# Optimization experiments

Hardware: AMD Instinct MI355X
Metric: run time of the kernel (lower is better)

The kernel has to match this reference:

```python
import jax, jax.numpy as jnp
import numpy as np

B, F, P = 16384, 4096, 32
D = F // P
EPS = 1e-5


def setup_inputs() -> dict:
    key = jax.random.key(0)
    ks = jax.random.split(key, 5)
    bound = 1.0 / np.sqrt(D)
    return {
        "x": jax.random.normal(ks[0], (B, F), dtype=jnp.float32),
        "weights1": jax.random.uniform(ks[1], (P, D, D), dtype=jnp.float32, minval=-bound, maxval=bound),
        "bias1": jax.random.uniform(ks[2], (F,), dtype=jnp.float32, minval=-bound, maxval=bound),
        "weights2": jax.random.uniform(ks[3], (P, D, D), dtype=jnp.float32, minval=-bound, maxval=bound),
        "bias2": jax.random.uniform(ks[4], (F,), dtype=jnp.float32, minval=-bound, maxval=bound),
        "gamma1": jnp.ones((F,), dtype=jnp.float32),
        "beta1": jnp.zeros((F,), dtype=jnp.float32),
        "gamma3": jnp.ones((F,), dtype=jnp.float32),
        "beta3": jnp.zeros((F,), dtype=jnp.float32),
    }


def _block_matmul(x, w):
    # x: [B, F] viewed as [B, P, D]; w: [P, D, D] block-diagonal blocks.
    # Equivalent to x @ block_diag(*w) without building the [F, F] matrix.
    xb = x.reshape(x.shape[0], P, D)
    return jnp.einsum("bpd,pde->bpe", xb, w).reshape(x.shape[0], F)


def _batchnorm(y, gamma, beta):
    # Training-mode BatchNorm1d: biased variance over the batch dim.
    mean = jnp.mean(y, axis=0)
    var = jnp.var(y, axis=0)
    return gamma * (y - mean) * jax.lax.rsqrt(var + EPS) + beta


def reference(x, weights1, bias1, weights2, bias2, gamma1, beta1, gamma3, beta3):
    o1 = jnp.tanh(_batchnorm(_block_matmul(x, weights1) + bias1, gamma1, beta1))
    o2 = _block_matmul(o1, weights2) + bias2
    o3 = jnp.tanh(_batchnorm(o2 + x, gamma3, beta3))
    return o3
```

## Files before the change

### kernel.cpp

```cpp
#include <hip/hip_runtime.h>
#include <hip/hip_bf16.h>
#include <cstdint>
#include <cstddef>

#define B_ 16384
#define F_ 4096
#define P_ 32
#define D_ 128
#define STRIPS 32
#define ITERS 8

using f32x4 = __attribute__((ext_vector_type(4))) float;
using s16x8 = __attribute__((ext_vector_type(8))) short;

union abuf { s16x8 v; uint32_t u[4]; };

__device__ inline uint32_t pk_bf16(float a, float b) {
    float2 f; f.x = a; f.y = b;
    union { __hip_bfloat162 h; uint32_t u; } cv;
    cv.h = __float22bfloat162_rn(f);
    return cv.u;
}
__device__ inline unsigned short bf16_rn1(float f) {
    union { float f; uint32_t u; } v; v.f = f;
    return (unsigned short)((v.u + 0x7FFFu + ((v.u >> 16) & 1u)) >> 16);
}
__device__ inline float bf16_f32(unsigned short h) {
    union { uint32_t u; float f; } v; v.u = ((uint32_t)h) << 16;
    return v.f;
}
__device__ inline float tanh_e(float ze) {
    float e = __builtin_amdgcn_exp2f(ze);
    return 1.f - 2.f * __builtin_amdgcn_rcpf(e + 1.f);
}

__device__ inline void stage_w(const float* __restrict__ Wp, short* s_w, int tid) {
#pragma unroll
    for (int it = 0; it < 8; ++it) {
        int slot = it * 256 + tid;
        int l15 = slot & 15;
        int l4  = (slot >> 4) & 3;
        int s   = (slot >> 6) & 3;
        int j   = slot >> 8;
        const float* src = Wp + (size_t)(s * 32 + l4 * 8) * D_ + j * 16 + l15;
        abuf a;
#pragma unroll
        for (int q = 0; q < 4; ++q) {
            float w0 = src[(size_t)(2 * q) * D_];
            float w1 = src[(size_t)(2 * q + 1) * D_];
            a.u[q] = pk_bf16(w0, w1);
        }
        *(s16x8*)((char*)s_w + (size_t)slot * 16) = a.v;
    }
}

template<bool OB>
__global__ __launch_bounds__(256, 4) void k_gemm1(
    const float* __restrict__ x, const float* __restrict__ W1,
    float* __restrict__ y1f, unsigned short* __restrict__ y1h,
    float* __restrict__ gsum, float* __restrict__ gsq)
{
    __shared__ short s_w[D_ * D_];
    __shared__ float s_sum[D_], s_sq[D_];
    const int tid = threadIdx.x;
    const int p = blockIdx.x / STRIPS;
    const int strip = blockIdx.x % STRIPS;
    stage_w(W1 + (size_t)p * D_ * D_, s_w, tid);
    if (tid < D_) { s_sum[tid] = 0.f; s_sq[tid] = 0.f; }
    __syncthreads();

    const int wave = tid >> 6, lane = tid & 63;
    const int l15 = lane & 15, l4 = lane >> 4;
    const int ldsb = lane * 16;

    float csum[8], csq[8];
#pragma unroll
    for (int j = 0; j < 8; ++j) { csum[j] = 0.f; csq[j] = 0.f; }

    for (int it = 0; it < ITERS; ++it) {
        const int row0 = strip * (ITERS * 64) + it * 64 + wave * 16;
        const float* ap = x + (size_t)(row0 + l15) * F_ + p * D_ + l4 * 8;
        f32x4 v[4][2];
#pragma unroll
        for (int s = 0; s < 4; ++s) {
            v[s][0] = *(const f32x4*)(ap + s * 32);
            v[s][1] = *(const f32x4*)(ap + s * 32 + 4);
        }
        abuf a[4];
#pragma unroll
        for (int s = 0; s < 4; ++s) {
            a[s].u[0] = pk_bf16(v[s][0][0], v[s][0][1]);
            a[s].u[1] = pk_bf16(v[s][0][2], v[s][0][3]);
            a[s].u[2] = pk_bf16(v[s][1][0], v[s][1][1]);
            a[s].u[3] = pk_bf16(v[s][1][2], v[s][1][3]);
        }
        f32x4 acc[8];
#pragma unroll
        for (int j = 0; j < 8; ++j) acc[j] = (f32x4){0.f, 0.f, 0.f, 0.f};
#pragma unroll
        for (int s = 0; s < 4; ++s)
#pragma unroll
            for (int j = 0; j < 8; ++j) {
                s16x8 b = *(const s16x8*)((const char*)s_w + (j * 4 + s) * 1024 + ldsb);
                acc[j] = __builtin_amdgcn_mfma_f32_16x16x32_bf16(a[s].v, b, acc[j], 0, 0, 0);
            }
        const int rb = row0 + l4 * 4;
#pragma unroll
        for (int j = 0; j < 8; ++j) {
            const size_t off = (size_t)rb * F_ + p * D_ + j * 16 + l15;
#pragma unroll
            for (int r = 0; r < 4; ++r) {
                float vv = acc[j][r];
                if (OB) y1h[off + (size_t)r * F_] = bf16_rn1(vv);
                else    y1f[off + (size_t)r * F_] = vv;
                csum[j] += vv;
                csq[j] = fmaf(vv, vv, csq[j]);
            }
        }
    }
#pragma unroll
    for (int j = 0; j < 8; ++j) {
        float sm = csum[j], q = csq[j];
        sm += __shfl_xor(sm, 16); q += __shfl_xor(q, 16);
        sm += __shfl_xor(sm, 32); q += __shfl_xor(q, 32);
        if (l4 == 0) {
            atomicAdd(&s_sum[j * 16 + l15], sm);
            atomicAdd(&s_sq[j * 16 + l15], q);
        }
    }
    __syncthreads();
    if (tid < D_) {
        atomicAdd(&gsum[p * D_ + tid], s_sum[tid]);
        atomicAdd(&gsq[p * D_ + tid], s_sq[tid]);
    }
}

template<bool IOB>
__global__ __launch_bounds__(256, 4) void k_gemm2(
    const float* __restrict__ x, float* __restrict__ yf,
    unsigned short* __restrict__ yh, const float* __restrict__ W2,
    const float* __restrict__ sce, const float* __restrict__ she,
    float* __restrict__ gsum, float* __restrict__ gsq)
{
    __shared__ short s_w[D_ * D_];
    __shared__ float s_sc[D_], s_sh[D_];
    __shared__ float s_sum[D_], s_sq[D_];
    const int tid = threadIdx.x;
    const int p = blockIdx.x / STRIPS;
    const int strip = blockIdx.x % STRIPS;
    stage_w(W2 + (size_t)p * D_ * D_, s_w, tid);
    if (tid < D_) {
        s_sc[tid] = sce[p * D_ + tid];
        s_sh[tid] = she[p * D_ + tid];
        s_sum[tid] = 0.f; s_sq[tid] = 0.f;
    }
    __syncthreads();

    const int wave = tid >> 6, lane = tid & 63;
    const int l15 = lane & 15, l4 = lane >> 4;
    const int ldsb = lane * 16;

    float csum[8], csq[8];
#pragma unroll
    for (int j = 0; j < 8; ++j) { csum[j] = 0.f; csq[j] = 0.f; }

    for (int it = 0; it < ITERS; ++it) {
        const int row0 = strip * (ITERS * 64) + it * 64 + wave * 16;
        s16x8 hv[4];
        f32x4 v[4][2];
        if (IOB) {
            const unsigned short* ap = yh + (size_t)(row0 + l15) * F_ + p * D_ + l4 * 8;
#pragma unroll
            for (int s = 0; s < 4; ++s) hv[s] = *(const s16x8*)(ap + s * 32);
        } else {
            const float* ap = yf + (size_t)(row0 + l15) * F_ + p * D_ + l4 * 8;
#pragma unroll
            for (int s = 0; s < 4; ++s) {
                v[s][0] = *(const f32x4*)(ap + s * 32);
                v[s][1] = *(const f32x4*)(ap + s * 32 + 4);
            }
        }
        abuf a[4];
#pragma unroll
        for (int s = 0; s < 4; ++s) {
            const int kb = s * 32 + l4 * 8;
            f32x4 sc0 = *(const f32x4*)&s_sc[kb];
            f32x4 sc1 = *(const f32x4*)&s_sc[kb + 4];
            f32x4 sh0 = *(const f32x4*)&s_sh[kb];
            f32x4 sh1 = *(const f32x4*)&s_sh[kb + 4];
            float t[8];
#pragma unroll
            for (int q = 0; q < 4; ++q) {
                float i0 = IOB ? bf16_f32((unsigned short)hv[s][q])     : v[s][0][q];
                float i1 = IOB ? bf16_f32((unsigned short)hv[s][q + 4]) : v[s][1][q];
                t[q]     = tanh_e(fmaf(i0, sc0[q], sh0[q]));
                t[q + 4] = tanh_e(fmaf(i1, sc1[q], sh1[q]));
            }
            a[s].u[0] = pk_bf16(t[0], t[1]);
            a[s].u[1] = pk_bf16(t[2], t[3]);
            a[s].u[2] = pk_bf16(t[4], t[5]);
            a[s].u[3] = pk_bf16(t[6], t[7]);
        }
        f32x4 acc[8];
#pragma unroll
        for (int j = 0; j < 8; ++j) acc[j] = (f32x4){0.f, 0.f, 0.f, 0.f};
#pragma unroll
        for (int s = 0; s < 4; ++s)
#pragma unroll
            for (int j = 0; j < 8; ++j) {
                s16x8 b = *(const s16x8*)((const char*)s_w + (j * 4 + s) * 1024 + ldsb);
                acc[j] = __builtin_amdgcn_mfma_f32_16x16x32_bf16(a[s].v, b, acc[j], 0, 0, 0);
            }
        const int rb = row0 + l4 * 4;
#pragma unroll
        for (int j = 0; j < 8; ++j) {
            const size_t off = (size_t)rb * F_ + p * D_ + j * 16 + l15;
#pragma unroll
            for (int r = 0; r < 4; ++r) {
                float vv = acc[j][r] + x[off + (size_t)r * F_];
                if (IOB) yh[off + (size_t)r * F_] = bf16_rn1(vv);
                else     yf[off + (size_t)r * F_] = vv;
                csum[j] += vv;
                csq[j] = fmaf(vv, vv, csq[j]);
            }
        }
    }
#pragma unroll
    for (int j = 0; j < 8; ++j) {
        float sm = csum[j], q = csq[j];
        sm += __shfl_xor(sm, 16); q += __shfl_xor(q, 16);
        sm += __shfl_xor(sm, 32); q += __shfl_xor(q, 32);
        if (l4 == 0) {
            atomicAdd(&s_sum[j * 16 + l15], sm);
            atomicAdd(&s_sq[j * 16 + l15], q);
        }
    }
    __syncthreads();
    if (tid < D_) {
        atomicAdd(&gsum[p * D_ + tid], s_sum[tid]);
        atomicAdd(&gsq[p * D_ + tid], s_sq[tid]);
    }
}

__global__ void k_finalize(const float* __restrict__ sum,
                           const float* __restrict__ sumsq,
                           const float* __restrict__ gamma,
                           const float* __restrict__ beta,
                           float* __restrict__ sce,
                           float* __restrict__ she)
{
    const float L2E2 = 2.f * 1.44269504088896340736f;
    int f = blockIdx.x * blockDim.x + threadIdx.x;
    if (f < F_) {
        float mean = sum[f] * (1.f / B_);
        float var  = sumsq[f] * (1.f / B_) - mean * mean;
        float rstd = rsqrtf(var + 1e-5f);
        float sc = gamma[f] * rstd;
        sce[f] = L2E2 * sc;
        she[f] = L2E2 * (beta[f] - mean * sc);
    }
}

template<bool IB>
__global__ void k_bn_tanh(const unsigned short* __restrict__ y3h,
                          float* __restrict__ outf,
                          const float* __restrict__ sce,
                          const float* __restrict__ she)
{
    if (IB) {
        const size_t n8 = (size_t)B_ * F_ / 8;
        size_t i = (size_t)blockIdx.x * blockDim.x + threadIdx.x;
        const size_t stride = (size_t)gridDim.x * blockDim.x;
        for (; i < n8; i += stride) {
            s16x8 hv = ((const s16x8*)y3h)[i];
            int col = (int)((i * 8) & (F_ - 1));
            f32x4 sc0 = *(const f32x4*)(sce + col);
            f32x4 sc1 = *(const f32x4*)(sce + col + 4);
            f32x4 sh0 = *(const f32x4*)(she + col);
            f32x4 sh1 = *(const f32x4*)(she + col + 4);
            f32x4 r0, r1;
#pragma unroll
            for (int t = 0; t < 4; ++t) {
                r0[t] = tanh_e(fmaf(bf16_f32((unsigned short)hv[t]),     sc0[t], sh0[t]));
                r1[t] = tanh_e(fmaf(bf16_f32((unsigned short)hv[t + 4]), sc1[t], sh1[t]));
            }
            ((f32x4*)outf)[i * 2]     = r0;
            ((f32x4*)outf)[i * 2 + 1] = r1;
        }
    } else {
        const size_t n4 = (size_t)B_ * F_ / 4;
        size_t i = (size_t)blockIdx.x * blockDim.x + threadIdx.x;
        const size_t stride = (size_t)gridDim.x * blockDim.x;
        for (; i < n4; i += stride) {
            f32x4 v = ((const f32x4*)outf)[i];
            int col = (int)((i * 4) & (F_ - 1));
            f32x4 sc = *(const f32x4*)(sce + col);
            f32x4 sh = *(const f32x4*)(she + col);
            f32x4 r;
#pragma unroll
            for (int t = 0; t < 4; ++t) r[t] = tanh_e(fmaf(v[t], sc[t], sh[t]));
            ((f32x4*)outf)[i] = r;
        }
    }
}

extern "C" void kernel_launch(void* const* d_in, const int* in_sizes, int n_in,
                              void* d_out, int out_size, void* d_ws, size_t ws_size,
                              hipStream_t stream) {
    const float* x      = (const float*)d_in[0];
    const float* W1     = (const float*)d_in[1];
    const float* W2     = (const float*)d_in[3];
    const float* gamma1 = (const float*)d_in[5];
    const float* beta1  = (const float*)d_in[6];
    const float* gamma3 = (const float*)d_in[7];
    const float* beta3  = (const float*)d_in[8];

    float* yf = (float*)d_out;
    float* S  = (float*)d_ws;
    float* sum1   = S;
    float* sumsq1 = S + 4096;
    float* sum3   = S + 8192;
    float* sumsq3 = S + 12288;
    float* sce1   = S + 16384;
    float* she1   = S + 20480;
    float* sce3   = S + 24576;
    float* she3   = S + 28672;
    unsigned short* yh = (unsigned short*)((char*)d_ws + 128 * 1024);

    const bool big = ws_size >= (size_t)128 * 1024 + (size_t)B_ * F_ * 2;

    hipMemsetAsync(d_ws, 0, 4 * 4096 * sizeof(float), stream);

    if (big) {
        k_gemm1<true><<<P_ * STRIPS, 256, 0, stream>>>(x, W1, yf, yh, sum1, sumsq1);
        k_finalize<<<F_ / 256, 256, 0, stream>>>(sum1, sumsq1, gamma1, beta1, sce1, she1);
        k_gemm2<true><<<P_ * STRIPS, 256, 0, stream>>>(x, yf, yh, W2, sce1, she1, sum3, sumsq3);
        k_finalize<<<F_ / 256, 256, 0, stream>>>(sum3, sumsq3, gamma3, beta3, sce3, she3);
        k_bn_tanh<true><<<2048, 256, 0, stream>>>(yh, yf, sce3, she3);
    } else {
        k_gemm1<false><<<P_ * STRIPS, 256, 0, stream>>>(x, W1, yf, yh, sum1, sumsq1);
        k_finalize<<<F_ / 256, 256, 0, stream>>>(sum1, sumsq1, gamma1, beta1, sce1, she1);
        k_gemm2<false><<<P_ * STRIPS, 256, 0, stream>>>(x, yf, yh, W2, sce1, she1, sum3, sumsq3);
        k_finalize<<<F_ / 256, 256, 0, stream>>>(sum3, sumsq3, gamma3, beta3, sce3, she3);
        k_bn_tanh<false><<<2048, 256, 0, stream>>>(yh, yf, sce3, she3);
    }
}
```

Measured before the change: 655.6 us.

## Store intermediates in MFMA-fragment tiled bf16 layout and move BN stats to separate kernel

The GEMM kernels now swap MFMA operand order so each lane holds four contiguous output columns. Intermediate bf16 activations are written as whole 16-byte fragments in a tiled layout that the next GEMM reads back directly, replacing the scattered 2-byte strided stores. The per-column sum and sum-of-squares reductions are removed from the GEMM epilogues and computed by a new dedicated stats kernel that re-reads the intermediate. This adds two launches and an extra pass over the intermediate, but in exchange gives coalesced, vectorized stores and lighter GEMM epilogues.

```diff
diff --git a/kernel.cpp b/kernel.cpp
--- a/kernel.cpp
+++ b/kernel.cpp
@@ -21,10 +21,6 @@
     cv.h = __float22bfloat162_rn(f);
     return cv.u;
 }
-__device__ inline unsigned short bf16_rn1(float f) {
-    union { float f; uint32_t u; } v; v.f = f;
-    return (unsigned short)((v.u + 0x7FFFu + ((v.u >> 16) & 1u)) >> 16);
-}
 __device__ inline float bf16_f32(unsigned short h) {
     union { uint32_t u; float f; } v; v.u = ((uint32_t)h) << 16;
     return v.f;
@@ -34,7 +30,7 @@
     return 1.f - 2.f * __builtin_amdgcn_rcpf(e + 1.f);
 }
 
-__device__ inline void stage_w(const float* __restrict__ Wp, short* s_w, int tid) {
+__device__ inline void stage_w1(const float* __restrict__ Wp, short* s_w, int tid) {
 #pragma unroll
     for (int it = 0; it < 8; ++it) {
         int slot = it * 256 + tid;
@@ -45,54 +41,63 @@
         const float* src = Wp + (size_t)(s * 32 + l4 * 8) * D_ + j * 16 + l15;
         abuf a;
 #pragma unroll
-        for (int q = 0; q < 4; ++q) {
-            float w0 = src[(size_t)(2 * q) * D_];
-            float w1 = src[(size_t)(2 * q + 1) * D_];
-            a.u[q] = pk_bf16(w0, w1);
-        }
+        for (int q = 0; q < 4; ++q)
+            a.u[q] = pk_bf16(src[(size_t)(2 * q) * D_], src[(size_t)(2 * q + 1) * D_]);
         *(s16x8*)((char*)s_w + (size_t)slot * 16) = a.v;
     }
 }
 
-template<bool OB>
+__device__ inline void stage_w2(const float* __restrict__ Wp, short* s_w, int tid) {
+#pragma unroll
+    for (int it = 0; it < 8; ++it) {
+        int slot = it * 256 + tid;
+        int l15 = slot & 15;
+        int l4  = (slot >> 4) & 3;
+        int sp  = (slot >> 6) & 3;
+        int j   = slot >> 8;
+        const float* s0 = Wp + (size_t)(sp * 32 + l4 * 4) * D_ + j * 16 + l15;
+        const float* s1 = s0 + (size_t)16 * D_;
+        abuf a;
+        a.u[0] = pk_bf16(s0[0],            s0[(size_t)D_]);
+        a.u[1] = pk_bf16(s0[(size_t)2*D_], s0[(size_t)3*D_]);
+        a.u[2] = pk_bf16(s1[0],            s1[(size_t)D_]);
+        a.u[3] = pk_bf16(s1[(size_t)2*D_], s1[(size_t)3*D_]);
+        *(s16x8*)((char*)s_w + (size_t)slot * 16) = a.v;
+    }
+}
+
+
+template<bool BH>
 __global__ __launch_bounds__(256, 4) void k_gemm1(
     const float* __restrict__ x, const float* __restrict__ W1,
-    float* __restrict__ y1f, unsigned short* __restrict__ y1h,
-    float* __restrict__ gsum, float* __restrict__ gsq)
+    float* __restrict__ yf, unsigned short* __restrict__ yh)
 {
     __shared__ short s_w[D_ * D_];
-    __shared__ float s_sum[D_], s_sq[D_];
     const int tid = threadIdx.x;
-    const int p = blockIdx.x / STRIPS;
-    const int strip = blockIdx.x % STRIPS;
-    stage_w(W1 + (size_t)p * D_ * D_, s_w, tid);
-    if (tid < D_) { s_sum[tid] = 0.f; s_sq[tid] = 0.f; }
+    const int p = blockIdx.x / STRIPS, strip = blockIdx.x % STRIPS;
+    stage_w1(W1 + (size_t)p * D_ * D_, s_w, tid);
     __syncthreads();
-
     const int wave = tid >> 6, lane = tid & 63;
     const int l15 = lane & 15, l4 = lane >> 4;
     const int ldsb = lane * 16;
 
-    float csum[8], csq[8];
-#pragma unroll
-    for (int j = 0; j < 8; ++j) { csum[j] = 0.f; csq[j] = 0.f; }
-
     for (int it = 0; it < ITERS; ++it) {
-        const int row0 = strip * (ITERS * 64) + it * 64 + wave * 16;
-        const float* ap = x + (size_t)(row0 + l15) * F_ + p * D_ + l4 * 8;
-        f32x4 v[4][2];
+        const int g = strip * 32 + it * 4 + wave;
+        const int row = g * 16 + l15;
+        const float* ap = x + (size_t)row * F_ + p * D_ + l4 * 8;
+        f32x4 v0[4], v1[4];
 #pragma unroll
         for (int s = 0; s < 4; ++s) {
-            v[s][0] = *(const f32x4*)(ap + s * 32);
-            v[s][1] = *(const f32x4*)(ap + s * 32 + 4);
+            v0[s] = *(const f32x4*)(ap + s * 32);
+            v1[s] = *(const f32x4*)(ap + s * 32 + 4);
         }
         abuf a[4];
 #pragma unroll
         for (int s = 0; s < 4; ++s) {
-            a[s].u[0] = pk_bf16(v[s][0][0], v[s][0][1]);
-            a[s].u[1] = pk_bf16(v[s][0][2], v[s][0][3]);
-            a[s].u[2] = pk_bf16(v[s][1][0], v[s][1][1]);
-            a[s].u[3] = pk_bf16(v[s][1][2], v[s][1][3]);
+            a[s].u[0] = pk_bf16(v0[s][0], v0[s][1]);
+            a[s].u[1] = pk_bf16(v0[s][2], v0[s][3]);
+            a[s].u[2] = pk_bf16(v1[s][0], v1[s][1]);
+            a[s].u[3] = pk_bf16(v1[s][2], v1[s][3]);
         }
         f32x4 acc[8];
 #pragma unroll
@@ -101,144 +106,182 @@
         for (int s = 0; s < 4; ++s)
 #pragma unroll
             for (int j = 0; j < 8; ++j) {
-                s16x8 b = *(const s16x8*)((const char*)s_w + (j * 4 + s) * 1024 + ldsb);
-                acc[j] = __builtin_amdgcn_mfma_f32_16x16x32_bf16(a[s].v, b, acc[j], 0, 0, 0);
-            }
-        const int rb = row0 + l4 * 4;
-#pragma unroll
-        for (int j = 0; j < 8; ++j) {
-            const size_t off = (size_t)rb * F_ + p * D_ + j * 16 + l15;
-#pragma unroll
-            for (int r = 0; r < 4; ++r) {
-                float vv = acc[j][r];
-                if (OB) y1h[off + (size_t)r * F_] = bf16_rn1(vv);
-                else    y1f[off + (size_t)r * F_] = vv;
-                csum[j] += vv;
-                csq[j] = fmaf(vv, vv, csq[j]);
-            }
-        }
-    }
-#pragma unroll
-    for (int j = 0; j < 8; ++j) {
-        float sm = csum[j], q = csq[j];
-        sm += __shfl_xor(sm, 16); q += __shfl_xor(q, 16);
-        sm += __shfl_xor(sm, 32); q += __shfl_xor(q, 32);
-        if (l4 == 0) {
-            atomicAdd(&s_sum[j * 16 + l15], sm);
-            atomicAdd(&s_sq[j * 16 + l15], q);
-        }
-    }
-    __syncthreads();
-    if (tid < D_) {
-        atomicAdd(&gsum[p * D_ + tid], s_sum[tid]);
-        atomicAdd(&gsq[p * D_ + tid], s_sq[tid]);
-    }
-}
-
-template<bool IOB>
+                s16x8 w = *(const s16x8*)((const char*)s_w + (j * 4 + s) * 1024 + ldsb);
+                acc[j] = __builtin_amdgcn_mfma_f32_16x16x32_bf16(w, a[s].v, acc[j], 0, 0, 0);
+            }
+        if (BH) {
+            unsigned short* tp = yh + ((size_t)g * 32 + p) * 2048 + lane * 8;
+#pragma unroll
+            for (int jp = 0; jp < 4; ++jp) {
+                abuf o;
+                o.u[0] = pk_bf16(acc[2*jp][0],   acc[2*jp][1]);
+                o.u[1] = pk_bf16(acc[2*jp][2],   acc[2*jp][3]);
+                o.u[2] = pk_bf16(acc[2*jp+1][0], acc[2*jp+1][1]);
+                o.u[3] = pk_bf16(acc[2*jp+1][2], acc[2*jp+1][3]);
+                *(s16x8*)(tp + jp * 512) = o.v;
+            }
+        } else {
+            float* rp = yf + (size_t)row * F_ + p * D_ + l4 * 4;
+#pragma unroll
+            for (int j = 0; j < 8; ++j) *(f32x4*)(rp + j * 16) = acc[j];
+        }
+    }
+}
+
+template<bool BH>
 __global__ __launch_bounds__(256, 4) void k_gemm2(
     const float* __restrict__ x, float* __restrict__ yf,
     unsigned short* __restrict__ yh, const float* __restrict__ W2,
-    const float* __restrict__ sce, const float* __restrict__ she,
-    float* __restrict__ gsum, float* __restrict__ gsq)
+    const float* __restrict__ sce, const float* __restrict__ she)
 {
     __shared__ short s_w[D_ * D_];
     __shared__ float s_sc[D_], s_sh[D_];
-    __shared__ float s_sum[D_], s_sq[D_];
     const int tid = threadIdx.x;
-    const int p = blockIdx.x / STRIPS;
-    const int strip = blockIdx.x % STRIPS;
-    stage_w(W2 + (size_t)p * D_ * D_, s_w, tid);
+    const int p = blockIdx.x / STRIPS, strip = blockIdx.x % STRIPS;
+    stage_w2(W2 + (size_t)p * D_ * D_, s_w, tid);
     if (tid < D_) {
         s_sc[tid] = sce[p * D_ + tid];
         s_sh[tid] = she[p * D_ + tid];
-        s_sum[tid] = 0.f; s_sq[tid] = 0.f;
     }
     __syncthreads();
-
     const int wave = tid >> 6, lane = tid & 63;
     const int l15 = lane & 15, l4 = lane >> 4;
     const int ldsb = lane * 16;
 
-    float csum[8], csq[8];
-#pragma unroll
-    for (int j = 0; j < 8; ++j) { csum[j] = 0.f; csq[j] = 0.f; }
-
     for (int it = 0; it < ITERS; ++it) {
-        const int row0 = strip * (ITERS * 64) + it * 64 + wave * 16;
-        s16x8 hv[4];
-        f32x4 v[4][2];
-        if (IOB) {
-            const unsigned short* ap = yh + (size_t)(row0 + l15) * F_ + p * D_ + l4 * 8;
-#pragma unroll
-            for (int s = 0; s < 4; ++s) hv[s] = *(const s16x8*)(ap + s * 32);
+        const int g = strip * 32 + it * 4 + wave;
+        const int row = g * 16 + l15;
+        abuf a[4];
+        if (BH) {
+            const unsigned short* tp = yh + ((size_t)g * 32 + p) * 2048 + lane * 8;
+            s16x8 hv[4];
+#pragma unroll
+            for (int sp = 0; sp < 4; ++sp) hv[sp] = *(const s16x8*)(tp + sp * 512);
+#pragma unroll
+            for (int sp = 0; sp < 4; ++sp) {
+                const int kb = sp * 32 + l4 * 4;
+                f32x4 sc0 = *(const f32x4*)&s_sc[kb], sc1 = *(const f32x4*)&s_sc[kb + 16];
+                f32x4 sh0 = *(const f32x4*)&s_sh[kb], sh1 = *(const f32x4*)&s_sh[kb + 16];
+                float t0[4], t1[4];
+#pragma unroll
+                for (int q = 0; q < 4; ++q) {
+                    t0[q] = tanh_e(fmaf(bf16_f32((unsigned short)hv[sp][q]),     sc0[q], sh0[q]));
+                    t1[q] = tanh_e(fmaf(bf16_f32((unsigned short)hv[sp][q + 4]), sc1[q], sh1[q]));
+                }
+                a[sp].u[0] = pk_bf16(t0[0], t0[1]);
+                a[sp].u[1] = pk_bf16(t0[2], t0[3]);
+                a[sp].u[2] = pk_bf16(t1[0], t1[1]);
+                a[sp].u[3] = pk_bf16(t1[2], t1[3]);
+            }
         } else {
-            const float* ap = yf + (size_t)(row0 + l15) * F_ + p * D_ + l4 * 8;
-#pragma unroll
-            for (int s = 0; s < 4; ++s) {
-                v[s][0] = *(const f32x4*)(ap + s * 32);
-                v[s][1] = *(const f32x4*)(ap + s * 32 + 4);
-            }
-        }
-        abuf a[4];
-#pragma unroll
-        for (int s = 0; s < 4; ++s) {
-            const int kb = s * 32 + l4 * 8;
-            f32x4 sc0 = *(const f32x4*)&s_sc[kb];
-            f32x4 sc1 = *(const f32x4*)&s_sc[kb + 4];
-            f32x4 sh0 = *(const f32x4*)&s_sh[kb];
-            f32x4 sh1 = *(const f32x4*)&s_sh[kb + 4];
-            float t[8];
-#pragma unroll
-            for (int q = 0; q < 4; ++q) {
-                float i0 = IOB ? bf16_f32((unsigned short)hv[s][q])     : v[s][0][q];
-                float i1 = IOB ? bf16_f32((unsigned short)hv[s][q + 4]) : v[s][1][q];
-                t[q]     = tanh_e(fmaf(i0, sc0[q], sh0[q]));
-                t[q + 4] = tanh_e(fmaf(i1, sc1[q], sh1[q]));
-            }
-            a[s].u[0] = pk_bf16(t[0], t[1]);
-            a[s].u[1] = pk_bf16(t[2], t[3]);
-            a[s].u[2] = pk_bf16(t[4], t[5]);
-            a[s].u[3] = pk_bf16(t[6], t[7]);
+            const float* ap = yf + (size_t)row * F_ + p * D_;
+#pragma unroll
+            for (int sp = 0; sp < 4; ++sp) {
+                const int kb = sp * 32 + l4 * 4;
+                f32x4 w0 = *(const f32x4*)(ap + kb);
+                f32x4 w1 = *(const f32x4*)(ap + kb + 16);
+                f32x4 sc0 = *(const f32x4*)&s_sc[kb], sc1 = *(const f32x4*)&s_sc[kb + 16];
+                f32x4 sh0 = *(const f32x4*)&s_sh[kb], sh1 = *(const f32x4*)&s_sh[kb + 16];
+                float t0[4], t1[4];
+#pragma unroll
+                for (int q = 0; q < 4; ++q) {
+                    t0[q] = tanh_e(fmaf(w0[q], sc0[q], sh0[q]));
+                    t1[q] = tanh_e(fmaf(w1[q], sc1[q], sh1[q]));
+                }
+                a[sp].u[0] = pk_bf16(t0[0], t0[1]);
+                a[sp].u[1] = pk_bf16(t0[2], t0[3]);
+                a[sp].u[2] = pk_bf16(t1[0], t1[1]);
+                a[sp].u[3] = pk_bf16(t1[2], t1[3]);
+            }
         }
         f32x4 acc[8];
 #pragma unroll
         for (int j = 0; j < 8; ++j) acc[j] = (f32x4){0.f, 0.f, 0.f, 0.f};
 #pragma unroll
-        for (int s = 0; s < 4; ++s)
+        for (int sp = 0; sp < 4; ++sp)
 #pragma unroll
             for (int j = 0; j < 8; ++j) {
-                s16x8 b = *(const s16x8*)((const char*)s_w + (j * 4 + s) * 1024 + ldsb);
-                acc[j] = __builtin_amdgcn_mfma_f32_16x16x32_bf16(a[s].v, b, acc[j], 0, 0, 0);
-            }
-        const int rb = row0 + l4 * 4;
+                s16x8 w = *(const s16x8*)((const char*)s_w + (j * 4 + sp) * 1024 + ldsb);
+                acc[j] = __builtin_amdgcn_mfma_f32_16x16x32_bf16(w, a[sp].v, acc[j], 0, 0, 0);
+            }
+        const float* xp = x + (size_t)row * F_ + p * D_ + l4 * 4;
 #pragma unroll
         for (int j = 0; j < 8; ++j) {
-            const size_t off = (size_t)rb * F_ + p * D_ + j * 16 + l15;
-#pragma unroll
-            for (int r = 0; r < 4; ++r) {
-                float vv = acc[j][r] + x[off + (size_t)r * F_];
-                if (IOB) yh[off + (size_t)r * F_] = bf16_rn1(vv);
-                else     yf[off + (size_t)r * F_] = vv;
-                csum[j] += vv;
-                csq[j] = fmaf(vv, vv, csq[j]);
-            }
-        }
-    }
-#pragma unroll
-    for (int j = 0; j < 8; ++j) {
-        float sm = csum[j], q = csq[j];
-        sm += __shfl_xor(sm, 16); q += __shfl_xor(q, 16);
-        sm += __shfl_xor(sm, 32); q += __shfl_xor(q, 32);
-        if (l4 == 0) {
-            atomicAdd(&s_sum[j * 16 + l15], sm);
-            atomicAdd(&s_sq[j * 16 + l15], q);
-        }
-    }
-    __syncthreads();
-    if (tid < D_) {
-        atomicAdd(&gsum[p * D_ + tid], s_sum[tid]);
-        atomicAdd(&gsq[p * D_ + tid], s_sq[tid]);
+            f32x4 xr = *(const f32x4*)(xp + j * 16);
+#pragma unroll
+            for (int r = 0; r < 4; ++r) acc[j][r] += xr[r];
+        }
+        if (BH) {
+            unsigned short* tp = yh + ((size_t)g * 32 + p) * 2048 + lane * 8;
+#pragma unroll
+            for (int jp = 0; jp < 4; ++jp) {
+                abuf o;
+                o.u[0] = pk_bf16(acc[2*jp][0],   acc[2*jp][1]);
+                o.u[1] = pk_bf16(acc[2*jp][2],   acc[2*jp][3]);
+                o.u[2] = pk_bf16(acc[2*jp+1][0], acc[2*jp+1][1]);
+                o.u[3] = pk_bf16(acc[2*jp+1][2], acc[2*jp+1][3]);
+                *(s16x8*)(tp + jp * 512) = o.v;
+            }
+        } else {
+            float* rp = yf + (size_t)row * F_ + p * D_ + l4 * 4;
+#pragma unroll
+            for (int j = 0; j < 8; ++j) *(f32x4*)(rp + j * 16) = acc[j];
+        }
+    }
+}
+
+template<bool BH>
+__global__ void k_stats(const float* __restrict__ yf,
+                        const unsigned short* __restrict__ yh,
+                        float* __restrict__ gsum, float* __restrict__ gsq)
+{
+    if (BH) {
+        const int tid = threadIdx.x;
+        const int p = blockIdx.x & 31, seg = blockIdx.x >> 5;
+        const int jp = tid >> 6, l4 = (tid >> 4) & 3, l15 = tid & 15;
+        const unsigned short* base = yh + (size_t)p * 2048 + jp * 512 + (l4 * 16 + l15) * 8;
+        float cs[8], cq[8];
+#pragma unroll
+        for (int t = 0; t < 8; ++t) { cs[t] = 0.f; cq[t] = 0.f; }
+        for (int g = seg * 128; g < seg * 128 + 128; ++g) {
+            s16x8 hv = *(const s16x8*)(base + (size_t)g * 65536);
+#pragma unroll
+            for (int t = 0; t < 8; ++t) {
+                float f = bf16_f32((unsigned short)hv[t]);
+                cs[t] += f; cq[t] = fmaf(f, f, cq[t]);
+            }
+        }
+#pragma unroll
+        for (int t = 0; t < 8; ++t) {
+            cs[t] += __shfl_xor(cs[t], 1); cq[t] += __shfl_xor(cq[t], 1);
+            cs[t] += __shfl_xor(cs[t], 2); cq[t] += __shfl_xor(cq[t], 2);
+            cs[t] += __shfl_xor(cs[t], 4); cq[t] += __shfl_xor(cq[t], 4);
+            cs[t] += __shfl_xor(cs[t], 8); cq[t] += __shfl_xor(cq[t], 8);
+        }
+        if (l15 == 0) {
+#pragma unroll
+            for (int t = 0; t < 8; ++t) {
+                int c = p * 128 + jp * 32 + (t >= 4 ? 16 : 0) + l4 * 4 + (t & 3);
+                atomicAdd(&gsum[c], cs[t]);
+                atomicAdd(&gsq[c],  cq[t]);
+            }
+        }
+    } else {
+        const int id = blockIdx.x * 256 + threadIdx.x;
+        const int c4 = id & 1023;
+        const int r0 = id >> 10;
+        const float* bp = yf + (size_t)r0 * F_ + c4 * 4;
+        f32x4 cs = {0.f,0.f,0.f,0.f}, cq = {0.f,0.f,0.f,0.f};
+        for (int k = 0; k < 64; ++k) {
+            f32x4 v = *(const f32x4*)(bp + (size_t)k * 256 * F_);
+#pragma unroll
+            for (int t = 0; t < 4; ++t) { cs[t] += v[t]; cq[t] = fmaf(v[t], v[t], cq[t]); }
+        }
+#pragma unroll
+        for (int t = 0; t < 4; ++t) {
+            atomicAdd(&gsum[c4 * 4 + t], cs[t]);
+            atomicAdd(&gsq[c4 * 4 + t],  cq[t]);
+        }
     }
 }
 
@@ -246,8 +289,7 @@
                            const float* __restrict__ sumsq,
                            const float* __restrict__ gamma,
                            const float* __restrict__ beta,
-                           float* __restrict__ sce,
-                           float* __restrict__ she)
+                           float* __restrict__ sce, float* __restrict__ she)
 {
     const float L2E2 = 2.f * 1.44269504088896340736f;
     int f = blockIdx.x * blockDim.x + threadIdx.x;
@@ -261,45 +303,49 @@
     }
 }
 
-template<bool IB>
-__global__ void k_bn_tanh(const unsigned short* __restrict__ y3h,
-                          float* __restrict__ outf,
+template<bool BH>
+__global__ void k_bn_tanh(const unsigned short* __restrict__ yh,
+                          float* __restrict__ out,
                           const float* __restrict__ sce,
                           const float* __restrict__ she)
 {
-    if (IB) {
-        const size_t n8 = (size_t)B_ * F_ / 8;
-        size_t i = (size_t)blockIdx.x * blockDim.x + threadIdx.x;
+    if (BH) {
+        const size_t NU = (size_t)B_ / 16 * P_ * 256;
+        size_t idx = (size_t)blockIdx.x * blockDim.x + threadIdx.x;
         const size_t stride = (size_t)gridDim.x * blockDim.x;
-        for (; i < n8; i += stride) {
-            s16x8 hv = ((const s16x8*)y3h)[i];
-            int col = (int)((i * 8) & (F_ - 1));
-            f32x4 sc0 = *(const f32x4*)(sce + col);
-            f32x4 sc1 = *(const f32x4*)(sce + col + 4);
-            f32x4 sh0 = *(const f32x4*)(she + col);
-            f32x4 sh1 = *(const f32x4*)(she + col + 4);
+        for (; idx < NU; idx += stride) {
+            s16x8 hv = *(const s16x8*)(yh + idx * 8);
+            int g = (int)(idx >> 13);
+            int rem = (int)(idx & 8191);
+            int p = rem >> 8, s = rem & 255;
+            int jp = s >> 6, l4 = (s >> 4) & 3, l15 = s & 15;
+            int c0 = p * 128 + jp * 32 + l4 * 4;
+            int row = g * 16 + l15;
+            f32x4 sc0 = *(const f32x4*)(sce + c0), sc1 = *(const f32x4*)(sce + c0 + 16);
+            f32x4 sh0 = *(const f32x4*)(she + c0), sh1 = *(const f32x4*)(she + c0 + 16);
             f32x4 r0, r1;
 #pragma unroll
             for (int t = 0; t < 4; ++t) {
                 r0[t] = tanh_e(fmaf(bf16_f32((unsigned short)hv[t]),     sc0[t], sh0[t]));
                 r1[t] = tanh_e(fmaf(bf16_f32((unsigned short)hv[t + 4]), sc1[t], sh1[t]));
             }
-            ((f32x4*)outf)[i * 2]     = r0;
-            ((f32x4*)outf)[i * 2 + 1] = r1;
+            float* op = out + (size_t)row * F_ + c0;
+            *(f32x4*)op = r0;
+            *(f32x4*)(op + 16) = r1;
         }
     } else {
         const size_t n4 = (size_t)B_ * F_ / 4;
         size_t i = (size_t)blockIdx.x * blockDim.x + threadIdx.x;
         const size_t stride = (size_t)gridDim.x * blockDim.x;
         for (; i < n4; i += stride) {
-            f32x4 v = ((const f32x4*)outf)[i];
+            f32x4 v = ((const f32x4*)out)[i];
             int col = (int)((i * 4) & (F_ - 1));
             f32x4 sc = *(const f32x4*)(sce + col);
             f32x4 sh = *(const f32x4*)(she + col);
             f32x4 r;
 #pragma unroll
             for (int t = 0; t < 4; ++t) r[t] = tanh_e(fmaf(v[t], sc[t], sh[t]));
-            ((f32x4*)outf)[i] = r;
+            ((f32x4*)out)[i] = r;
         }
     }
 }
@@ -318,9 +364,9 @@
     float* yf = (float*)d_out;
     float* S  = (float*)d_ws;
     float* sum1   = S;
-    float* sumsq1 = S + 4096;
+    float* sq1    = S + 4096;
     float* sum3   = S + 8192;
-    float* sumsq3 = S + 12288;
+    float* sq3    = S + 12288;
     float* sce1   = S + 16384;
     float* she1   = S + 20480;
     float* sce3   = S + 24576;
@@ -332,16 +378,20 @@
     hipMemsetAsync(d_ws, 0, 4 * 4096 * sizeof(float), stream);
 
     if (big) {
-        k_gemm1<true><<<P_ * STRIPS, 256, 0, stream>>>(x, W1, yf, yh, sum1, sumsq1);
-        k_finalize<<<F_ / 256, 256, 0, stream>>>(sum1, sumsq1, gamma1, beta1, sce1, she1);
-        k_gemm2<true><<<P_ * STRIPS, 256, 0, stream>>>(x, yf, yh, W2, sce1, she1, sum3, sumsq3);
-        k_finalize<<<F_ / 256, 256, 0, stream>>>(sum3, sumsq3, gamma3, beta3, sce3, she3);
-        k_bn_tanh<true><<<2048, 256, 0, stream>>>(yh, yf, sce3, she3);
+        k_gemm1<true><<<P_ * STRIPS, 256, 0, stream>>>(x, W1, yf, yh);
+        k_stats<true><<<256, 256, 0, stream>>>(yf, yh, sum1, sq1);
+        k_finalize<<<F_ / 256, 256, 0, stream>>>(sum1, sq1, gamma1, beta1, sce1, she1);
+        k_gemm2<true><<<P_ * STRIPS, 256, 0, stream>>>(x, yf, yh, W2, sce1, she1);
+        k_stats<true><<<256, 256, 0, stream>>>(yf, yh, sum3, sq3);
+        k_finalize<<<F_ / 256, 256, 0, stream>>>(sum3, sq3, gamma3, beta3, sce3, she3);
+        k_bn_tanh<true><<<8192, 256, 0, stream>>>(yh, yf, sce3, she3);
     } else {
-        k_gemm1<false><<<P_ * STRIPS, 256, 0, stream>>>(x, W1, yf, yh, sum1, sumsq1);
-        k_finalize<<<F_ / 256, 256, 0, stream>>>(sum1, sumsq1, gamma1, beta1, sce1, she1);
-        k_gemm2<false><<<P_ * STRIPS, 256, 0, stream>>>(x, yf, yh, W2, sce1, she1, sum3, sumsq3);
-        k_finalize<<<F_ / 256, 256, 0, stream>>>(sum3, sumsq3, gamma3, beta3, sce3, she3);
-        k_bn_tanh<false><<<2048, 256, 0, stream>>>(yh, yf, sce3, she3);
-    }
-}
+        k_gemm1<false><<<P_ * STRIPS, 256, 0, stream>>>(x, W1, yf, yh);
+        k_stats<false><<<1024, 256, 0, stream>>>(yf, yh, sum1, sq1);
+        k_finalize<<<F_ / 256, 256, 0, stream>>>(sum1, sq1, gamma1, beta1, sce1, she1);
+        k_gemm2<false><<<P_ * STRIPS, 256, 0, stream>>>(x, yf, yh, W2, sce1, she1);
+        k_stats<false><<<1024, 256, 0, stream>>>(yf, yh, sum3, sq3);
+        k_finalize<<<F_ / 256, 256, 0, stream>>>(sum3, sq3, gamma3, beta3, sce3, she3);
+        k_bn_tanh<false><<<4096, 256, 0, stream>>>(yh, yf, sce3, she3);
+    }
+}
```

Result: faster. 530.9 us (-19.0%).

## Recompute first GEMM in fused kernel instead of storing intermediate activations

Applied to the files above, without the earlier changes.

The first pass now only computes BN1 statistics and no longer writes the y1 intermediate. A fused kernel recomputes x@W1, applies BN1 and tanh in registers, then runs the second GEMM with transposed MFMA operands so accumulator outputs feed straight into the next A operand. It also adds the residual from the x already loaded. This trades an extra GEMM's compute for removing a full-size intermediate write and read, and drops the bf16 workspace path. Nontemporal loads and stores plus double-buffered x loads are added, and occupancy drops because two weight tiles now sit in LDS.

```diff
diff --git a/kernel.cpp b/kernel.cpp
--- a/kernel.cpp
+++ b/kernel.cpp
@@ -21,224 +21,228 @@
     cv.h = __float22bfloat162_rn(f);
     return cv.u;
 }
-__device__ inline unsigned short bf16_rn1(float f) {
-    union { float f; uint32_t u; } v; v.f = f;
-    return (unsigned short)((v.u + 0x7FFFu + ((v.u >> 16) & 1u)) >> 16);
-}
-__device__ inline float bf16_f32(unsigned short h) {
-    union { uint32_t u; float f; } v; v.u = ((uint32_t)h) << 16;
-    return v.f;
-}
 __device__ inline float tanh_e(float ze) {
     float e = __builtin_amdgcn_exp2f(ze);
     return 1.f - 2.f * __builtin_amdgcn_rcpf(e + 1.f);
 }
 
-__device__ inline void stage_w(const float* __restrict__ Wp, short* s_w, int tid) {
+__device__ inline void stage_wp(const float* __restrict__ Wp, short* s_w, int tid) {
 #pragma unroll
     for (int it = 0; it < 8; ++it) {
         int slot = it * 256 + tid;
         int l15 = slot & 15;
         int l4  = (slot >> 4) & 3;
-        int s   = (slot >> 6) & 3;
+        int sp  = (slot >> 6) & 3;
         int j   = slot >> 8;
-        const float* src = Wp + (size_t)(s * 32 + l4 * 8) * D_ + j * 16 + l15;
+        const float* s0 = Wp + (size_t)(sp * 32 + l4 * 4) * D_ + j * 16 + l15;
+        const float* s1 = s0 + (size_t)16 * D_;
         abuf a;
-#pragma unroll
-        for (int q = 0; q < 4; ++q) {
-            float w0 = src[(size_t)(2 * q) * D_];
-            float w1 = src[(size_t)(2 * q + 1) * D_];
-            a.u[q] = pk_bf16(w0, w1);
-        }
+        a.u[0] = pk_bf16(s0[0],            s0[(size_t)D_]);
+        a.u[1] = pk_bf16(s0[(size_t)2*D_], s0[(size_t)3*D_]);
+        a.u[2] = pk_bf16(s1[0],            s1[(size_t)D_]);
+        a.u[3] = pk_bf16(s1[(size_t)2*D_], s1[(size_t)3*D_]);
         *(s16x8*)((char*)s_w + (size_t)slot * 16) = a.v;
     }
 }
 
-template<bool OB>
-__global__ __launch_bounds__(256, 4) void k_gemm1(
+__global__ __launch_bounds__(256, 3) void k_stats1(
     const float* __restrict__ x, const float* __restrict__ W1,
-    float* __restrict__ y1f, unsigned short* __restrict__ y1h,
     float* __restrict__ gsum, float* __restrict__ gsq)
 {
     __shared__ short s_w[D_ * D_];
     __shared__ float s_sum[D_], s_sq[D_];
     const int tid = threadIdx.x;
-    const int p = blockIdx.x / STRIPS;
-    const int strip = blockIdx.x % STRIPS;
-    stage_w(W1 + (size_t)p * D_ * D_, s_w, tid);
+    const int p = blockIdx.x / STRIPS, strip = blockIdx.x % STRIPS;
+    stage_wp(W1 + (size_t)p * D_ * D_, s_w, tid);
     if (tid < D_) { s_sum[tid] = 0.f; s_sq[tid] = 0.f; }
     __syncthreads();
-
     const int wave = tid >> 6, lane = tid & 63;
     const int l15 = lane & 15, l4 = lane >> 4;
     const int ldsb = lane * 16;
 
-    float csum[8], csq[8];
-#pragma unroll
-    for (int j = 0; j < 8; ++j) { csum[j] = 0.f; csq[j] = 0.f; }
+    f32x4 csum[8], csq[8];
+#pragma unroll
+    for (int j = 0; j < 8; ++j) { csum[j] = (f32x4){0,0,0,0}; csq[j] = (f32x4){0,0,0,0}; }
 
     for (int it = 0; it < ITERS; ++it) {
-        const int row0 = strip * (ITERS * 64) + it * 64 + wave * 16;
-        const float* ap = x + (size_t)(row0 + l15) * F_ + p * D_ + l4 * 8;
-        f32x4 v[4][2];
+        const int g = strip * 32 + it * 4 + wave;
+        const float* ap = x + (size_t)(g * 16 + l15) * F_ + p * D_ + l4 * 4;
+        f32x4 xv[8];
+#pragma unroll
+        for (int j = 0; j < 8; ++j)
+            xv[j] = __builtin_nontemporal_load((const f32x4*)(ap + j * 16));
+        abuf a[4];
 #pragma unroll
         for (int s = 0; s < 4; ++s) {
-            v[s][0] = *(const f32x4*)(ap + s * 32);
-            v[s][1] = *(const f32x4*)(ap + s * 32 + 4);
-        }
-        abuf a[4];
-#pragma unroll
-        for (int s = 0; s < 4; ++s) {
-            a[s].u[0] = pk_bf16(v[s][0][0], v[s][0][1]);
-            a[s].u[1] = pk_bf16(v[s][0][2], v[s][0][3]);
-            a[s].u[2] = pk_bf16(v[s][1][0], v[s][1][1]);
-            a[s].u[3] = pk_bf16(v[s][1][2], v[s][1][3]);
+            a[s].u[0] = pk_bf16(xv[2*s][0],   xv[2*s][1]);
+            a[s].u[1] = pk_bf16(xv[2*s][2],   xv[2*s][3]);
+            a[s].u[2] = pk_bf16(xv[2*s+1][0], xv[2*s+1][1]);
+            a[s].u[3] = pk_bf16(xv[2*s+1][2], xv[2*s+1][3]);
         }
         f32x4 acc[8];
 #pragma unroll
-        for (int j = 0; j < 8; ++j) acc[j] = (f32x4){0.f, 0.f, 0.f, 0.f};
+        for (int j = 0; j < 8; ++j) acc[j] = (f32x4){0,0,0,0};
 #pragma unroll
         for (int s = 0; s < 4; ++s)
 #pragma unroll
             for (int j = 0; j < 8; ++j) {
-                s16x8 b = *(const s16x8*)((const char*)s_w + (j * 4 + s) * 1024 + ldsb);
-                acc[j] = __builtin_amdgcn_mfma_f32_16x16x32_bf16(a[s].v, b, acc[j], 0, 0, 0);
-            }
-        const int rb = row0 + l4 * 4;
-#pragma unroll
-        for (int j = 0; j < 8; ++j) {
-            const size_t off = (size_t)rb * F_ + p * D_ + j * 16 + l15;
+                s16x8 w = *(const s16x8*)((const char*)s_w + (j * 4 + s) * 1024 + ldsb);
+                acc[j] = __builtin_amdgcn_mfma_f32_16x16x32_bf16(w, a[s].v, acc[j], 0, 0, 0);
+            }
+#pragma unroll
+        for (int j = 0; j < 8; ++j)
 #pragma unroll
             for (int r = 0; r < 4; ++r) {
-                float vv = acc[j][r];
-                if (OB) y1h[off + (size_t)r * F_] = bf16_rn1(vv);
-                else    y1f[off + (size_t)r * F_] = vv;
-                csum[j] += vv;
-                csq[j] = fmaf(vv, vv, csq[j]);
-            }
-        }
-    }
-#pragma unroll
-    for (int j = 0; j < 8; ++j) {
-        float sm = csum[j], q = csq[j];
-        sm += __shfl_xor(sm, 16); q += __shfl_xor(q, 16);
-        sm += __shfl_xor(sm, 32); q += __shfl_xor(q, 32);
-        if (l4 == 0) {
-            atomicAdd(&s_sum[j * 16 + l15], sm);
-            atomicAdd(&s_sq[j * 16 + l15], q);
-        }
-    }
+                float v = acc[j][r];
+                csum[j][r] += v;
+                csq[j][r] = fmaf(v, v, csq[j][r]);
+            }
+    }
+#pragma unroll
+    for (int j = 0; j < 8; ++j)
+#pragma unroll
+        for (int r = 0; r < 4; ++r) {
+            float sm = csum[j][r], q = csq[j][r];
+            sm += __shfl_xor(sm, 1); q += __shfl_xor(q, 1);
+            sm += __shfl_xor(sm, 2); q += __shfl_xor(q, 2);
+            sm += __shfl_xor(sm, 4); q += __shfl_xor(q, 4);
+            sm += __shfl_xor(sm, 8); q += __shfl_xor(q, 8);
+            if (l15 == 0) {
+                atomicAdd(&s_sum[j * 16 + l4 * 4 + r], sm);
+                atomicAdd(&s_sq [j * 16 + l4 * 4 + r], q);
+            }
+        }
     __syncthreads();
     if (tid < D_) {
         atomicAdd(&gsum[p * D_ + tid], s_sum[tid]);
-        atomicAdd(&gsq[p * D_ + tid], s_sq[tid]);
-    }
-}
-
-template<bool IOB>
-__global__ __launch_bounds__(256, 4) void k_gemm2(
+        atomicAdd(&gsq [p * D_ + tid], s_sq[tid]);
+    }
+}
+
+__global__ __launch_bounds__(256, 2) void k_fused(
     const float* __restrict__ x, float* __restrict__ yf,
-    unsigned short* __restrict__ yh, const float* __restrict__ W2,
+    const float* __restrict__ W1, const float* __restrict__ W2,
     const float* __restrict__ sce, const float* __restrict__ she,
     float* __restrict__ gsum, float* __restrict__ gsq)
 {
-    __shared__ short s_w[D_ * D_];
+    __shared__ short s_w1[D_ * D_];
+    __shared__ short s_w2[D_ * D_];
     __shared__ float s_sc[D_], s_sh[D_];
     __shared__ float s_sum[D_], s_sq[D_];
     const int tid = threadIdx.x;
-    const int p = blockIdx.x / STRIPS;
-    const int strip = blockIdx.x % STRIPS;
-    stage_w(W2 + (size_t)p * D_ * D_, s_w, tid);
+    const int p = blockIdx.x / STRIPS, strip = blockIdx.x % STRIPS;
+    stage_wp(W1 + (size_t)p * D_ * D_, s_w1, tid);
+    stage_wp(W2 + (size_t)p * D_ * D_, s_w2, tid);
     if (tid < D_) {
         s_sc[tid] = sce[p * D_ + tid];
         s_sh[tid] = she[p * D_ + tid];
         s_sum[tid] = 0.f; s_sq[tid] = 0.f;
     }
     __syncthreads();
-
     const int wave = tid >> 6, lane = tid & 63;
     const int l15 = lane & 15, l4 = lane >> 4;
     const int ldsb = lane * 16;
 
-    float csum[8], csq[8];
-#pragma unroll
-    for (int j = 0; j < 8; ++j) { csum[j] = 0.f; csq[j] = 0.f; }
-
-    for (int it = 0; it < ITERS; ++it) {
-        const int row0 = strip * (ITERS * 64) + it * 64 + wave * 16;
-        s16x8 hv[4];
-        f32x4 v[4][2];
-        if (IOB) {
-            const unsigned short* ap = yh + (size_t)(row0 + l15) * F_ + p * D_ + l4 * 8;
-#pragma unroll
-            for (int s = 0; s < 4; ++s) hv[s] = *(const s16x8*)(ap + s * 32);
-        } else {
-            const float* ap = yf + (size_t)(row0 + l15) * F_ + p * D_ + l4 * 8;
-#pragma unroll
-            for (int s = 0; s < 4; ++s) {
-                v[s][0] = *(const f32x4*)(ap + s * 32);
-                v[s][1] = *(const f32x4*)(ap + s * 32 + 4);
-            }
-        }
+    f32x4 csum[8], csq[8];
+#pragma unroll
+    for (int j = 0; j < 8; ++j) { csum[j] = (f32x4){0,0,0,0}; csq[j] = (f32x4){0,0,0,0}; }
+
+    auto LOADX = [&](f32x4 (&xv)[8], int it) {
+        const int g = strip * 32 + it * 4 + wave;
+        const float* ap = x + (size_t)(g * 16 + l15) * F_ + p * D_ + l4 * 4;
+#pragma unroll
+        for (int j = 0; j < 8; ++j)
+            xv[j] = __builtin_nontemporal_load((const f32x4*)(ap + j * 16));
+    };
+
+    auto TILE = [&](f32x4 (&xv)[8], int it) {
         abuf a[4];
 #pragma unroll
         for (int s = 0; s < 4; ++s) {
-            const int kb = s * 32 + l4 * 8;
-            f32x4 sc0 = *(const f32x4*)&s_sc[kb];
-            f32x4 sc1 = *(const f32x4*)&s_sc[kb + 4];
-            f32x4 sh0 = *(const f32x4*)&s_sh[kb];
-            f32x4 sh1 = *(const f32x4*)&s_sh[kb + 4];
-            float t[8];
+            a[s].u[0] = pk_bf16(xv[2*s][0],   xv[2*s][1]);
+            a[s].u[1] = pk_bf16(xv[2*s][2],   xv[2*s][3]);
+            a[s].u[2] = pk_bf16(xv[2*s+1][0], xv[2*s+1][1]);
+            a[s].u[3] = pk_bf16(xv[2*s+1][2], xv[2*s+1][3]);
+        }
+        f32x4 acc[8];
+#pragma unroll
+        for (int j = 0; j < 8; ++j) acc[j] = (f32x4){0,0,0,0};
+#pragma unroll
+        for (int s = 0; s < 4; ++s)
+#pragma unroll
+            for (int j = 0; j < 8; ++j) {
+                s16x8 w = *(const s16x8*)((const char*)s_w1 + (j * 4 + s) * 1024 + ldsb);
+                acc[j] = __builtin_amdgcn_mfma_f32_16x16x32_bf16(w, a[s].v, acc[j], 0, 0, 0);
+            }
+#pragma unroll
+        for (int sp = 0; sp < 4; ++sp) {
+            const int kb = sp * 32 + l4 * 4;
+            f32x4 sc0 = *(const f32x4*)&s_sc[kb], sc1 = *(const f32x4*)&s_sc[kb + 16];
+            f32x4 sh0 = *(const f32x4*)&s_sh[kb], sh1 = *(const f32x4*)&s_sh[kb + 16];
+            float t0[4], t1[4];
 #pragma unroll
             for (int q = 0; q < 4; ++q) {
-                float i0 = IOB ? bf16_f32((unsigned short)hv[s][q])     : v[s][0][q];
-                float i1 = IOB ? bf16_f32((unsigned short)hv[s][q + 4]) : v[s][1][q];
-                t[q]     = tanh_e(fmaf(i0, sc0[q], sh0[q]));
-                t[q + 4] = tanh_e(fmaf(i1, sc1[q], sh1[q]));
-            }
-            a[s].u[0] = pk_bf16(t[0], t[1]);
-            a[s].u[1] = pk_bf16(t[2], t[3]);
-            a[s].u[2] = pk_bf16(t[4], t[5]);
-            a[s].u[3] = pk_bf16(t[6], t[7]);
-        }
-        f32x4 acc[8];
-#pragma unroll
-        for (int j = 0; j < 8; ++j) acc[j] = (f32x4){0.f, 0.f, 0.f, 0.f};
-#pragma unroll
-        for (int s = 0; s < 4; ++s)
+                t0[q] = tanh_e(fmaf(acc[2*sp][q],   sc0[q], sh0[q]));
+                t1[q] = tanh_e(fmaf(acc[2*sp+1][q], sc1[q], sh1[q]));
+            }
+            a[sp].u[0] = pk_bf16(t0[0], t0[1]);
+            a[sp].u[1] = pk_bf16(t0[2], t0[3]);
+            a[sp].u[2] = pk_bf16(t1[0], t1[1]);
+            a[sp].u[3] = pk_bf16(t1[2], t1[3]);
+        }
+#pragma unroll
+        for (int j = 0; j < 8; ++j) acc[j] = (f32x4){0,0,0,0};
+#pragma unroll
+        for (int sp = 0; sp < 4; ++sp)
 #pragma unroll
             for (int j = 0; j < 8; ++j) {
-                s16x8 b = *(const s16x8*)((const char*)s_w + (j * 4 + s) * 1024 + ldsb);
-                acc[j] = __builtin_amdgcn_mfma_f32_16x16x32_bf16(a[s].v, b, acc[j], 0, 0, 0);
-            }
-        const int rb = row0 + l4 * 4;
+                s16x8 w = *(const s16x8*)((const char*)s_w2 + (j * 4 + sp) * 1024 + ldsb);
+                acc[j] = __builtin_amdgcn_mfma_f32_16x16x32_bf16(w, a[sp].v, acc[j], 0, 0, 0);
+            }
+        const int g = strip * 32 + it * 4 + wave;
+        float* rp = yf + (size_t)(g * 16 + l15) * F_ + p * D_ + l4 * 4;
 #pragma unroll
         for (int j = 0; j < 8; ++j) {
-            const size_t off = (size_t)rb * F_ + p * D_ + j * 16 + l15;
+            f32x4 o;
 #pragma unroll
             for (int r = 0; r < 4; ++r) {
-                float vv = acc[j][r] + x[off + (size_t)r * F_];
-                if (IOB) yh[off + (size_t)r * F_] = bf16_rn1(vv);
-                else     yf[off + (size_t)r * F_] = vv;
-                csum[j] += vv;
-                csq[j] = fmaf(vv, vv, csq[j]);
-            }
-        }
-    }
-#pragma unroll
-    for (int j = 0; j < 8; ++j) {
-        float sm = csum[j], q = csq[j];
-        sm += __shfl_xor(sm, 16); q += __shfl_xor(q, 16);
-        sm += __shfl_xor(sm, 32); q += __shfl_xor(q, 32);
-        if (l4 == 0) {
-            atomicAdd(&s_sum[j * 16 + l15], sm);
-            atomicAdd(&s_sq[j * 16 + l15], q);
-        }
-    }
+                float v = acc[j][r] + xv[j][r];
+                o[r] = v;
+                csum[j][r] += v;
+                csq[j][r] = fmaf(v, v, csq[j][r]);
+            }
+            __builtin_nontemporal_store(o, (f32x4*)(rp + j * 16));
+        }
+    };
+
+    f32x4 xv0[8], xv1[8];
+    LOADX(xv0, 0);
+#pragma unroll
+    for (int h = 0; h < 4; ++h) {
+        LOADX(xv1, 2 * h + 1);
+        TILE(xv0, 2 * h);
+        if (h < 3) LOADX(xv0, 2 * h + 2);
+        TILE(xv1, 2 * h + 1);
+    }
+
+#pragma unroll
+    for (int j = 0; j < 8; ++j)
+#pragma unroll
+        for (int r = 0; r < 4; ++r) {
+            float sm = csum[j][r], q = csq[j][r];
+            sm += __shfl_xor(sm, 1); q += __shfl_xor(q, 1);
+            sm += __shfl_xor(sm, 2); q += __shfl_xor(q, 2);
+            sm += __shfl_xor(sm, 4); q += __shfl_xor(q, 4);
+            sm += __shfl_xor(sm, 8); q += __shfl_xor(q, 8);
+            if (l15 == 0) {
+                atomicAdd(&s_sum[j * 16 + l4 * 4 + r], sm);
+                atomicAdd(&s_sq [j * 16 + l4 * 4 + r], q);
+            }
+        }
     __syncthreads();
     if (tid < D_) {
         atomicAdd(&gsum[p * D_ + tid], s_sum[tid]);
-        atomicAdd(&gsq[p * D_ + tid], s_sq[tid]);
+        atomicAdd(&gsq [p * D_ + tid], s_sq[tid]);
     }
 }
 
@@ -246,8 +250,7 @@
                            const float* __restrict__ sumsq,
                            const float* __restrict__ gamma,
                            const float* __restrict__ beta,
-                           float* __restrict__ sce,
-                           float* __restrict__ she)
+                           float* __restrict__ sce, float* __restrict__ she)
 {
     const float L2E2 = 2.f * 1.44269504088896340736f;
     int f = blockIdx.x * blockDim.x + threadIdx.x;
@@ -261,46 +264,21 @@
     }
 }
 
-template<bool IB>
-__global__ void k_bn_tanh(const unsigned short* __restrict__ y3h,
-                          float* __restrict__ outf,
-                          const float* __restrict__ sce,
+__global__ void k_bn_tanh(float* yb, const float* __restrict__ sce,
                           const float* __restrict__ she)
 {
-    if (IB) {
-        const size_t n8 = (size_t)B_ * F_ / 8;
-        size_t i = (size_t)blockIdx.x * blockDim.x + threadIdx.x;
-        const size_t stride = (size_t)gridDim.x * blockDim.x;
-        for (; i < n8; i += stride) {
-            s16x8 hv = ((const s16x8*)y3h)[i];
-            int col = (int)((i * 8) & (F_ - 1));
-            f32x4 sc0 = *(const f32x4*)(sce + col);
-            f32x4 sc1 = *(const f32x4*)(sce + col + 4);
-            f32x4 sh0 = *(const f32x4*)(she + col);
-            f32x4 sh1 = *(const f32x4*)(she + col + 4);
-            f32x4 r0, r1;
-#pragma unroll
-            for (int t = 0; t < 4; ++t) {
-                r0[t] = tanh_e(fmaf(bf16_f32((unsigned short)hv[t]),     sc0[t], sh0[t]));
-                r1[t] = tanh_e(fmaf(bf16_f32((unsigned short)hv[t + 4]), sc1[t], sh1[t]));
-            }
-            ((f32x4*)outf)[i * 2]     = r0;
-            ((f32x4*)outf)[i * 2 + 1] = r1;
-        }
-    } else {
-        const size_t n4 = (size_t)B_ * F_ / 4;
-        size_t i = (size_t)blockIdx.x * blockDim.x + threadIdx.x;
-        const size_t stride = (size_t)gridDim.x * blockDim.x;
-        for (; i < n4; i += stride) {
-            f32x4 v = ((const f32x4*)outf)[i];
-            int col = (int)((i * 4) & (F_ - 1));
-            f32x4 sc = *(const f32x4*)(sce + col);
-            f32x4 sh = *(const f32x4*)(she + col);
-            f32x4 r;
-#pragma unroll
-            for (int t = 0; t < 4; ++t) r[t] = tanh_e(fmaf(v[t], sc[t], sh[t]));
-            ((f32x4*)outf)[i] = r;
-        }
+    const size_t n4 = (size_t)B_ * F_ / 4;
+    size_t i = (size_t)blockIdx.x * blockDim.x + threadIdx.x;
+    const size_t stride = (size_t)gridDim.x * blockDim.x;
+    for (; i < n4; i += stride) {
+        f32x4 v = __builtin_nontemporal_load((const f32x4*)yb + i);
+        int col = (int)((i * 4) & (F_ - 1));
+        f32x4 sc = *(const f32x4*)(sce + col);
+        f32x4 sh = *(const f32x4*)(she + col);
+        f32x4 r;
+#pragma unroll
+        for (int t = 0; t < 4; ++t) r[t] = tanh_e(fmaf(v[t], sc[t], sh[t]));
+        __builtin_nontemporal_store(r, (f32x4*)yb + i);
     }
 }
 
@@ -317,31 +295,20 @@
 
     float* yf = (float*)d_out;
     float* S  = (float*)d_ws;
-    float* sum1   = S;
-    float* sumsq1 = S + 4096;
-    float* sum3   = S + 8192;
-    float* sumsq3 = S + 12288;
-    float* sce1   = S + 16384;
-    float* she1   = S + 20480;
-    float* sce3   = S + 24576;
-    float* she3   = S + 28672;
-    unsigned short* yh = (unsigned short*)((char*)d_ws + 128 * 1024);
-
-    const bool big = ws_size >= (size_t)128 * 1024 + (size_t)B_ * F_ * 2;
+    float* sum1 = S;
+    float* sq1  = S + 4096;
+    float* sum3 = S + 8192;
+    float* sq3  = S + 12288;
+    float* sce1 = S + 16384;
+    float* she1 = S + 20480;
+    float* sce3 = S + 24576;
+    float* she3 = S + 28672;
 
     hipMemsetAsync(d_ws, 0, 4 * 4096 * sizeof(float), stream);
 
-    if (big) {
-        k_gemm1<true><<<P_ * STRIPS, 256, 0, stream>>>(x, W1, yf, yh, sum1, sumsq1);
-        k_finalize<<<F_ / 256, 256, 0, stream>>>(sum1, sumsq1, gamma1, beta1, sce1, she1);
-        k_gemm2<true><<<P_ * STRIPS, 256, 0, stream>>>(x, yf, yh, W2, sce1, she1, sum3, sumsq3);
-        k_finalize<<<F_ / 256, 256, 0, stream>>>(sum3, sumsq3, gamma3, beta3, sce3, she3);
-        k_bn_tanh<true><<<2048, 256, 0, stream>>>(yh, yf, sce3, she3);
-    } else {
-        k_gemm1<false><<<P_ * STRIPS, 256, 0, stream>>>(x, W1, yf, yh, sum1, sumsq1);
-        k_finalize<<<F_ / 256, 256, 0, stream>>>(sum1, sumsq1, gamma1, beta1, sce1, she1);
-        k_gemm2<false><<<P_ * STRIPS, 256, 0, stream>>>(x, yf, yh, W2, sce1, she1, sum3, sumsq3);
-        k_finalize<<<F_ / 256, 256, 0, stream>>>(sum3, sumsq3, gamma3, beta3, sce3, she3);
-        k_bn_tanh<false><<<2048, 256, 0, stream>>>(yh, yf, sce3, she3);
-    }
-}
+    k_stats1<<<P_ * STRIPS, 256, 0, stream>>>(x, W1, sum1, sq1);
+    k_finalize<<<F_ / 256, 256, 0, stream>>>(sum1, sq1, gamma1, beta1, sce1, she1);
+    k_fused<<<P_ * STRIPS, 256, 0, stream>>>(x, yf, W1, W2, sce1, she1, sum3, sq3);
+    k_finalize<<<F_ / 256, 256, 0, stream>>>(sum3, sq3, gamma3, beta3, sce3, she3);
+    k_bn_tanh<<<4096, 256, 0, stream>>>(yf, sce3, she3);
+}
```

After: 627.2 us. -4.3%, faster.
